# Performance work log

Measured on AMD Instinct MI355X. Metric: run time of the kernel, lower is better.

Reference implementation:

```python
import jax, jax.numpy as jnp
import numpy as np


def _step(state):
    # state: [B, H, W] in {0.0, 1.0}
    p = jnp.pad(state, ((0, 0), (1, 1), (1, 1)))
    neighbors = (p[:, :-2, :-2] + p[:, :-2, 1:-1] + p[:, :-2, 2:]
                 + p[:, 1:-1, :-2] + p[:, 1:-1, 2:]
                 + p[:, 2:, :-2] + p[:, 2:, 1:-1] + p[:, 2:, 2:])
    alive = state > 0.5
    survives = alive & ((neighbors == 2.0) | (neighbors == 3.0))
    born = (~alive) & (neighbors == 3.0)
    return jnp.where(survives | born, jnp.ones_like(state), jnp.zeros_like(state))


def setup_inputs() -> dict:
    key = jax.random.key(0)
    k1, k2 = jax.random.split(key)
    B, H, W = 32, 1024, 1024
    # Binary occupancy grids in {0.0, 1.0} as the rule expects
    initial_state = (jax.random.uniform(k1, (B, H, W)) > 0.5).astype(jnp.float32)
    target = (jax.random.uniform(k2, (B, H, W)) > 0.5).astype(jnp.float32)
    return {"initial_state": initial_state, "target": target, "generations": 8}


def reference(initial_state, target, generations):
    state = initial_state
    for _ in range(generations):  # small fixed unroll, strict sequential dependency
        state = _step(state)
    error = state - target
    loss = jnp.mean(error * error)
    live_cells = state.sum()
    max_abs_error = jnp.abs(error).max()
    return loss, state, target, live_cells, max_abs_error
```

## Files before the change

kernel.cpp:

```cpp
#include <hip/hip_runtime.h>
#include <cstdint>

typedef unsigned long long u64;
typedef float f4v __attribute__((ext_vector_type(4)));

#define BATCH   32
#define H       1024
#define W       1024
#define WPR     16
#define GENS    8
#define HALO    8
#define NTOT    33554432ULL
#define NROWS   (BATCH * H)

#define PK_THREADS 256
#define PK_WAVES   4
#define PK_ROWS_PER_BLOCK 32
#define PK_GRID    (NROWS / PK_ROWS_PER_BLOCK)

__device__ __forceinline__ u64 shflxor64(u64 v, int m) {
    return (u64)__shfl_xor((long long)v, m, 64);
}

__global__ __launch_bounds__(PK_THREADS)
void gol_pack(const float* __restrict__ in_state, u64* __restrict__ packed)
{
    const int tid  = threadIdx.x;
    const int wave = tid >> 6;
    const int lane = tid & 63;
    const int sub  = lane & 15;
    const int wsub = lane >> 4;

    const int row0 = blockIdx.x * PK_ROWS_PER_BLOCK;
    for (int rr = wave; rr < PK_ROWS_PER_BLOCK; rr += PK_WAVES) {
        int row = row0 + rr;
        const f4v* rowp4 = (const f4v*)(in_state + (size_t)row * W);
        u64* prow = packed + (size_t)row * WPR;
        #pragma unroll
        for (int g = 0; g < 4; ++g) {
            f4v f = __builtin_nontemporal_load(&rowp4[g * 64 + lane]);
            u64 nib = (u64)((f.x > 0.5f) | ((f.y > 0.5f) << 1) |
                            ((f.z > 0.5f) << 2) | ((f.w > 0.5f) << 3));
            u64 v = nib << (sub * 4);
            v |= shflxor64(v, 1);
            v |= shflxor64(v, 2);
            v |= shflxor64(v, 4);
            v |= shflxor64(v, 8);
            if (sub == 0)
                prow[g * 4 + wsub] = v;
        }
    }
}

#define TR      32
#define BR      (TR + 2*HALO)
#define BRP     (BR + 2)
#define WP      (WPR + 2)
#define LF_THREADS 256
#define LF_GRID (BATCH * (H / TR))

__global__ __launch_bounds__(LF_THREADS)
void gol_life(const u64* __restrict__ packedI, u64* __restrict__ packedO)
{
    __shared__ u64 buf[2][BRP][WP];

    const int tile = blockIdx.x;
    const int tpb  = H / TR;
    const int b    = tile / tpb;
    const int r0   = (tile - b * tpb) * TR;

    const int tid  = threadIdx.x;

    for (int i = tid; i < 2 * BRP * WP; i += LF_THREADS)
        ((u64*)buf)[i] = 0ULL;
    __syncthreads();

    const u64* packedb = packedI + (size_t)b * H * WPR;
    #pragma unroll
    for (int k = 0; k < (BR * WPR) / LF_THREADS; ++k) {
        int idx = tid + k * LF_THREADS;
        int br = idx >> 4;
        int c  = idx & 15;
        int gr = r0 - HALO + br;
        if (gr >= 0 && gr < H)
            buf[0][br + 1][c + 1] = packedb[(size_t)gr * WPR + c];
    }
    __syncthreads();

    int cur = 0;
    for (int step = 0; step < GENS; ++step) {
        #pragma unroll
        for (int k = 0; k < (BR * WPR) / LF_THREADS; ++k) {
            int idx = tid + k * LF_THREADS;
            int br = idx >> 4;
            int c  = (idx & 15) + 1;
            int r  = br + 1;
            int gr = r0 - HALO + br;

            u64 uL = buf[cur][r-1][c-1], uC = buf[cur][r-1][c], uR = buf[cur][r-1][c+1];
            u64 mL = buf[cur][r  ][c-1], mC = buf[cur][r  ][c], mR = buf[cur][r  ][c+1];
            u64 dL = buf[cur][r+1][c-1], dC = buf[cur][r+1][c], dR = buf[cur][r+1][c+1];

            u64 uw = (uC << 1) | (uL >> 63), ue = (uC >> 1) | (uR << 63);
            u64 mw = (mC << 1) | (mL >> 63), me = (mC >> 1) | (mR << 63);
            u64 dw = (dC << 1) | (dL >> 63), de = (dC >> 1) | (dR << 63);
            u64 o0 = uw ^ uC ^ ue, t0 = (uw & uC) | (ue & (uw ^ uC));
            u64 o1 = mw ^ mC ^ me, t1 = (mw & mC) | (me & (mw ^ mC));
            u64 o2 = dw ^ dC ^ de, t2 = (dw & dC) | (de & (dw ^ dC));

            u64 oa = o0 ^ o1 ^ o2;
            u64 oc = (o0 & o1) | (o2 & (o0 ^ o1));
            u64 ts = t0 ^ t1 ^ t2;
            u64 tc = (t0 & t1) | (t2 & (t0 ^ t1));
            u64 b1 = oc ^ ts;
            u64 cc = oc & ts;
            u64 b2 = cc ^ tc;
            u64 b3 = cc & tc;
            u64 eq3 = oa & b1 & ~(b2 | b3);
            u64 eq4 = (~oa) & (~b1) & b2 & (~b3);
            u64 nxtw = eq3 | (mC & eq4);

            buf[cur ^ 1][r][c] = (gr >= 0 && gr < H) ? nxtw : 0ULL;
        }
        __syncthreads();
        cur ^= 1;
    }

    const size_t Rbase = (size_t)b * H + r0;
    #pragma unroll
    for (int k = 0; k < (TR * WPR) / LF_THREADS; ++k) {
        int idx = tid + k * LF_THREADS;
        int lr = idx >> 4;
        int c  = idx & 15;
        packedO[(Rbase + lr) * WPR + c] = buf[cur][HALO + lr + 1][c + 1];
    }
}

#define UP_THREADS 256
#define UP_WAVES   4
#define RPB        32
#define UP_GRID    (NROWS / RPB)

__global__ __launch_bounds__(UP_THREADS)
void gol_unpack(const u64* __restrict__ packedS,
                const float* __restrict__ target,
                float* __restrict__ out,
                u64* __restrict__ counters)
{
    __shared__ u64 rows[RPB][WPR + 1];
    __shared__ unsigned int wsum[UP_WAVES];

    const int tid  = threadIdx.x;
    const int wave = tid >> 6;
    const int lane = tid & 63;
    const int R0   = blockIdx.x * RPB;

    #pragma unroll
    for (int k = 0; k < (RPB * WPR) / UP_THREADS; ++k) {
        int idx = tid + k * UP_THREADS;
        rows[idx >> 4][idx & 15] = packedS[(size_t)R0 * WPR + idx];
    }
    if (tid < RPB) rows[tid][WPR] = 0ULL;
    __syncthreads();

    float* o_state = out + 1;
    float* o_tgt   = out + 1 + NTOT;

    unsigned int mism = 0, live = 0;
    for (int lr = wave; lr < RPB; lr += UP_WAVES) {
        size_t rowbase = (size_t)(R0 + lr) * W;
        const u64* wrow = rows[lr];
        const float* trow = target + rowbase;
        float* osrow = o_state + rowbase;
        float* otrow = o_tgt + rowbase;
        #pragma unroll
        for (int g = 0; g < 4; ++g) {
            int k = g * 64 + lane;
            if (k < 255) {
                int bitbase = 4 * k + 3;
                int w0 = bitbase >> 6;
                int sh = bitbase & 63;
                u64 lo = wrow[w0];
                u64 hi = wrow[w0 + 1];
                unsigned bits = (unsigned)(((lo >> sh) | (hi << (64 - sh))) & 0xFULL);
                f4v t = __builtin_nontemporal_load((const f4v*)(trow + bitbase));
                unsigned tb = (unsigned)((t.x > 0.5f) | ((t.y > 0.5f) << 1) |
                                         ((t.z > 0.5f) << 2) | ((t.w > 0.5f) << 3));
                mism += (unsigned)__popc(bits ^ tb);
                live += (unsigned)__popc(bits);
                f4v sv;
                sv.x = (float)(bits & 1u);
                sv.y = (float)((bits >> 1) & 1u);
                sv.z = (float)((bits >> 2) & 1u);
                sv.w = (float)((bits >> 3) & 1u);
                __builtin_nontemporal_store(sv, (f4v*)(osrow + bitbase));
                __builtin_nontemporal_store(t,  (f4v*)(otrow + bitbase));
            } else {
                u64 wfirst = wrow[0];
                u64 wlast  = wrow[15];
                unsigned hb   = (unsigned)(wfirst & 7ULL);
                unsigned tbit = (unsigned)(wlast >> 63);
                float t0 = trow[0], t1 = trow[1], t2 = trow[2], t3 = trow[1023];
                unsigned htb = (unsigned)((t0 > 0.5f) | ((t1 > 0.5f) << 1) | ((t2 > 0.5f) << 2));
                unsigned ttb = (unsigned)(t3 > 0.5f);
                mism += (unsigned)__popc(hb ^ htb) + (tbit ^ ttb);
                live += (unsigned)__popc(hb) + tbit;
                __builtin_nontemporal_store((float)(hb & 1u),        osrow);
                __builtin_nontemporal_store((float)((hb >> 1) & 1u), osrow + 1);
                __builtin_nontemporal_store((float)((hb >> 2) & 1u), osrow + 2);
                __builtin_nontemporal_store((float)tbit,             osrow + 1023);
                __builtin_nontemporal_store(t0, otrow);
                __builtin_nontemporal_store(t1, otrow + 1);
                __builtin_nontemporal_store(t2, otrow + 2);
                __builtin_nontemporal_store(t3, otrow + 1023);
            }
        }
    }

    unsigned int comb = (mism << 16) | live;
    #pragma unroll
    for (int m = 1; m < 64; m <<= 1)
        comb += (unsigned int)__shfl_xor((int)comb, m, 64);
    if (lane == 0) wsum[wave] = comb;
    __syncthreads();

    if (tid == 0) {
        unsigned int bm = 0, bl = 0;
        #pragma unroll
        for (int i = 0; i < UP_WAVES; ++i) {
            bm += wsum[i] >> 16;
            bl += wsum[i] & 0xFFFFu;
        }
        atomicAdd(counters, ((u64)bm << 32) | (u64)bl);
    }
}

__global__ void gol_finalize(const u64* __restrict__ counters,
                             float* __restrict__ out)
{
    u64 c = *counters;
    unsigned int mism = (unsigned int)(c >> 32);
    unsigned int live = (unsigned int)(c & 0xFFFFFFFFULL);
    out[0]            = (float)((double)mism / (double)NTOT);
    out[1 + 2*NTOT]   = (float)live;
    out[2 + 2*NTOT]   = (mism > 0) ? 1.0f : 0.0f;
}

extern "C" void kernel_launch(void* const* d_in, const int* in_sizes, int n_in,
                              void* d_out, int out_size, void* d_ws, size_t ws_size,
                              hipStream_t stream) {
    (void)in_sizes; (void)n_in; (void)out_size; (void)ws_size;
    const float* in_state = (const float*)d_in[0];
    const float* target   = (const float*)d_in[1];
    float* out = (float*)d_out;

    u64* counters = (u64*)d_ws;
    u64* packedI  = (u64*)((char*)d_ws + 4096);
    u64* packedO  = (u64*)((char*)d_ws + 4096 + (4u << 20));

    hipMemsetAsync(d_ws, 0, sizeof(u64), stream);

    gol_pack  <<<dim3(PK_GRID), dim3(PK_THREADS), 0, stream>>>(in_state, packedI);
    gol_life  <<<dim3(LF_GRID), dim3(LF_THREADS), 0, stream>>>(packedI, packedO);
    gol_unpack<<<dim3(UP_GRID), dim3(UP_THREADS), 0, stream>>>(packedO, target, out, counters);
    gol_finalize<<<1, 1, 0, stream>>>(counters, out);
}
```

Before: 488.7 us.

## Drop nontemporal hints, shrink pack/unpack blocks, replace atomic with slot reduction

Pack and unpack kernels now process fewer rows per block (16 and 8), giving larger grids. Loads and stores switch from nontemporal builtins to plain accesses. Unpack reads packed words straight from global memory instead of staging them in LDS, so it needs no barrier. The global atomic plus memset is replaced by per-wave partial sums in slots, which a 256-thread finalize kernel reduces. The counter widens to 64 bits, which removes the 16-bit packing overflow risk, at the cost of a larger finalize pass and possibly different cache behaviour for the streaming traffic.

```diff
diff --git a/kernel.cpp b/kernel.cpp
--- a/kernel.cpp
+++ b/kernel.cpp
@@ -13,14 +13,14 @@
 #define NTOT    33554432ULL
 #define NROWS   (BATCH * H)
 
+__device__ __forceinline__ u64 shflxor64(u64 v, int m) {
+    return (u64)__shfl_xor((long long)v, m, 64);
+}
+
 #define PK_THREADS 256
 #define PK_WAVES   4
-#define PK_ROWS_PER_BLOCK 32
-#define PK_GRID    (NROWS / PK_ROWS_PER_BLOCK)
-
-__device__ __forceinline__ u64 shflxor64(u64 v, int m) {
-    return (u64)__shfl_xor((long long)v, m, 64);
-}
+#define PK_RPB     16
+#define PK_GRID    (NROWS / PK_RPB)
 
 __global__ __launch_bounds__(PK_THREADS)
 void gol_pack(const float* __restrict__ in_state, u64* __restrict__ packed)
@@ -31,14 +31,15 @@
     const int sub  = lane & 15;
     const int wsub = lane >> 4;
 
-    const int row0 = blockIdx.x * PK_ROWS_PER_BLOCK;
-    for (int rr = wave; rr < PK_ROWS_PER_BLOCK; rr += PK_WAVES) {
-        int row = row0 + rr;
+    const int row0 = blockIdx.x * PK_RPB;
+    #pragma unroll
+    for (int rr = 0; rr < PK_RPB / PK_WAVES; ++rr) {
+        int row = row0 + wave + rr * PK_WAVES;
         const f4v* rowp4 = (const f4v*)(in_state + (size_t)row * W);
         u64* prow = packed + (size_t)row * WPR;
         #pragma unroll
         for (int g = 0; g < 4; ++g) {
-            f4v f = __builtin_nontemporal_load(&rowp4[g * 64 + lane]);
+            f4v f = rowp4[g * 64 + lane];
             u64 nib = (u64)((f.x > 0.5f) | ((f.y > 0.5f) << 1) |
                             ((f.z > 0.5f) << 2) | ((f.w > 0.5f) << 3));
             u64 v = nib << (sub * 4);
@@ -138,38 +139,30 @@
 
 #define UP_THREADS 256
 #define UP_WAVES   4
-#define RPB        32
-#define UP_GRID    (NROWS / RPB)
+#define UP_RPB     8
+#define UP_GRID    (NROWS / UP_RPB)
+#define NSLOTS     (UP_GRID * UP_WAVES)
 
 __global__ __launch_bounds__(UP_THREADS)
 void gol_unpack(const u64* __restrict__ packedS,
                 const float* __restrict__ target,
                 float* __restrict__ out,
-                u64* __restrict__ counters)
-{
-    __shared__ u64 rows[RPB][WPR + 1];
-    __shared__ unsigned int wsum[UP_WAVES];
-
+                u64* __restrict__ slots)
+{
     const int tid  = threadIdx.x;
     const int wave = tid >> 6;
     const int lane = tid & 63;
-    const int R0   = blockIdx.x * RPB;
-
-    #pragma unroll
-    for (int k = 0; k < (RPB * WPR) / UP_THREADS; ++k) {
-        int idx = tid + k * UP_THREADS;
-        rows[idx >> 4][idx & 15] = packedS[(size_t)R0 * WPR + idx];
-    }
-    if (tid < RPB) rows[tid][WPR] = 0ULL;
-    __syncthreads();
+    const int R0   = blockIdx.x * UP_RPB;
 
     float* o_state = out + 1;
     float* o_tgt   = out + 1 + NTOT;
 
     unsigned int mism = 0, live = 0;
-    for (int lr = wave; lr < RPB; lr += UP_WAVES) {
-        size_t rowbase = (size_t)(R0 + lr) * W;
-        const u64* wrow = rows[lr];
+    #pragma unroll
+    for (int rr = 0; rr < UP_RPB / UP_WAVES; ++rr) {
+        int row = R0 + wave + rr * UP_WAVES;
+        size_t rowbase = (size_t)row * W;
+        const u64* wrow = packedS + (size_t)row * WPR;
         const float* trow = target + rowbase;
         float* osrow = o_state + rowbase;
         float* otrow = o_tgt + rowbase;
@@ -183,7 +176,7 @@
                 u64 lo = wrow[w0];
                 u64 hi = wrow[w0 + 1];
                 unsigned bits = (unsigned)(((lo >> sh) | (hi << (64 - sh))) & 0xFULL);
-                f4v t = __builtin_nontemporal_load((const f4v*)(trow + bitbase));
+                f4v t = *(const f4v*)(trow + bitbase);
                 unsigned tb = (unsigned)((t.x > 0.5f) | ((t.y > 0.5f) << 1) |
                                          ((t.z > 0.5f) << 2) | ((t.w > 0.5f) << 3));
                 mism += (unsigned)__popc(bits ^ tb);
@@ -193,8 +186,8 @@
                 sv.y = (float)((bits >> 1) & 1u);
                 sv.z = (float)((bits >> 2) & 1u);
                 sv.w = (float)((bits >> 3) & 1u);
-                __builtin_nontemporal_store(sv, (f4v*)(osrow + bitbase));
-                __builtin_nontemporal_store(t,  (f4v*)(otrow + bitbase));
+                *(f4v*)(osrow + bitbase) = sv;
+                *(f4v*)(otrow + bitbase) = t;
             } else {
                 u64 wfirst = wrow[0];
                 u64 wlast  = wrow[15];
@@ -205,45 +198,47 @@
                 unsigned ttb = (unsigned)(t3 > 0.5f);
                 mism += (unsigned)__popc(hb ^ htb) + (tbit ^ ttb);
                 live += (unsigned)__popc(hb) + tbit;
-                __builtin_nontemporal_store((float)(hb & 1u),        osrow);
-                __builtin_nontemporal_store((float)((hb >> 1) & 1u), osrow + 1);
-                __builtin_nontemporal_store((float)((hb >> 2) & 1u), osrow + 2);
-                __builtin_nontemporal_store((float)tbit,             osrow + 1023);
-                __builtin_nontemporal_store(t0, otrow);
-                __builtin_nontemporal_store(t1, otrow + 1);
-                __builtin_nontemporal_store(t2, otrow + 2);
-                __builtin_nontemporal_store(t3, otrow + 1023);
+                osrow[0] = (float)(hb & 1u);
+                osrow[1] = (float)((hb >> 1) & 1u);
+                osrow[2] = (float)((hb >> 2) & 1u);
+                osrow[1023] = (float)tbit;
+                otrow[0] = t0; otrow[1] = t1; otrow[2] = t2; otrow[1023] = t3;
             }
         }
     }
 
-    unsigned int comb = (mism << 16) | live;
+    u64 comb = ((u64)mism << 32) | (u64)live;
     #pragma unroll
     for (int m = 1; m < 64; m <<= 1)
-        comb += (unsigned int)__shfl_xor((int)comb, m, 64);
-    if (lane == 0) wsum[wave] = comb;
+        comb += (u64)__shfl_xor((long long)comb, m, 64);
+    if (lane == 0)
+        slots[blockIdx.x * UP_WAVES + wave] = comb;
+}
+
+__global__ __launch_bounds__(256)
+void gol_finalize(const u64* __restrict__ slots, float* __restrict__ out)
+{
+    __shared__ u64 wsum[4];
+    const int tid  = threadIdx.x;
+    const int wave = tid >> 6;
+    const int lane = tid & 63;
+
+    u64 s = 0;
+    for (int i = tid; i < NSLOTS; i += 256)
+        s += slots[i];
+    #pragma unroll
+    for (int m = 1; m < 64; m <<= 1)
+        s += (u64)__shfl_xor((long long)s, m, 64);
+    if (lane == 0) wsum[wave] = s;
     __syncthreads();
-
     if (tid == 0) {
-        unsigned int bm = 0, bl = 0;
-        #pragma unroll
-        for (int i = 0; i < UP_WAVES; ++i) {
-            bm += wsum[i] >> 16;
-            bl += wsum[i] & 0xFFFFu;
-        }
-        atomicAdd(counters, ((u64)bm << 32) | (u64)bl);
-    }
-}
-
-__global__ void gol_finalize(const u64* __restrict__ counters,
-                             float* __restrict__ out)
-{
-    u64 c = *counters;
-    unsigned int mism = (unsigned int)(c >> 32);
-    unsigned int live = (unsigned int)(c & 0xFFFFFFFFULL);
-    out[0]            = (float)((double)mism / (double)NTOT);
-    out[1 + 2*NTOT]   = (float)live;
-    out[2 + 2*NTOT]   = (mism > 0) ? 1.0f : 0.0f;
+        u64 tot = wsum[0] + wsum[1] + wsum[2] + wsum[3];
+        unsigned int mism = (unsigned int)(tot >> 32);
+        unsigned int live = (unsigned int)(tot & 0xFFFFFFFFULL);
+        out[0]            = (float)((double)mism / (double)NTOT);
+        out[1 + 2*NTOT]   = (float)live;
+        out[2 + 2*NTOT]   = (mism > 0) ? 1.0f : 0.0f;
+    }
 }
 
 extern "C" void kernel_launch(void* const* d_in, const int* in_sizes, int n_in,
@@ -254,14 +249,12 @@
     const float* target   = (const float*)d_in[1];
     float* out = (float*)d_out;
 
-    u64* counters = (u64*)d_ws;
-    u64* packedI  = (u64*)((char*)d_ws + 4096);
-    u64* packedO  = (u64*)((char*)d_ws + 4096 + (4u << 20));
-
-    hipMemsetAsync(d_ws, 0, sizeof(u64), stream);
-
-    gol_pack  <<<dim3(PK_GRID), dim3(PK_THREADS), 0, stream>>>(in_state, packedI);
-    gol_life  <<<dim3(LF_GRID), dim3(LF_THREADS), 0, stream>>>(packedI, packedO);
-    gol_unpack<<<dim3(UP_GRID), dim3(UP_THREADS), 0, stream>>>(packedO, target, out, counters);
-    gol_finalize<<<1, 1, 0, stream>>>(counters, out);
-}
+    u64* slots   = (u64*)d_ws;
+    u64* packedI = (u64*)((char*)d_ws + (1u << 20));
+    u64* packedO = (u64*)((char*)d_ws + (6u << 20));
+
+    gol_pack    <<<dim3(PK_GRID), dim3(PK_THREADS), 0, stream>>>(in_state, packedI);
+    gol_life    <<<dim3(LF_GRID), dim3(LF_THREADS), 0, stream>>>(packedI, packedO);
+    gol_unpack  <<<dim3(UP_GRID), dim3(UP_THREADS), 0, stream>>>(packedO, target, out, slots);
+    gol_finalize<<<1, 256, 0, stream>>>(slots, out);
+}
```

Result: no change. 494.5 us (+1.2%).
